# Optimization experiments

Measured on AMD Instinct MI355X. Metric: run time of the kernel, lower is better.

## Reference

```python
import jax, jax.numpy as jnp
import numpy as np

B, T, D = 4, 2048, 1024

def layer_norm(x, gamma, bias):
    # NOTE: faithfully reproduces the source's (buggy) LN: x - mu/sqrt(var), unbiased var
    mu = jnp.mean(x, axis=-1, keepdims=True)
    var = jnp.var(x, axis=-1, ddof=1, keepdims=True)
    return (x - mu / jnp.sqrt(var)) * gamma + bias

def setup_inputs() -> dict:
    key = jax.random.key(0)
    ks = jax.random.split(key, 8)
    scale = 1.0 / np.sqrt(D)
    return {
        'x': jax.random.normal(ks[0], (B, T, D), dtype=jnp.float32),
        'gamma1': jnp.ones((D,), jnp.float32),
        'beta1': jnp.zeros((D,), jnp.float32),
        'w_q': jax.random.uniform(ks[1], (D, D), jnp.float32, -scale, scale),
        'w_k': jax.random.uniform(ks[2], (D, D), jnp.float32, -scale, scale),
        'w_v': jax.random.uniform(ks[3], (D, D), jnp.float32, -scale, scale),
        'gamma2': jnp.ones((D,), jnp.float32),
        'beta2': jnp.zeros((D,), jnp.float32),
        'W1': jax.random.uniform(ks[4], (D, D), jnp.float32, -scale, scale),
        'b1': jnp.zeros((D,), jnp.float32),
        'W2': jax.random.uniform(ks[5], (D, D), jnp.float32, -scale, scale),
        'b2': jnp.zeros((D,), jnp.float32),
    }

def reference(x, gamma1, beta1, w_q, w_k, w_v, gamma2, beta2, W1, b1, W2, b2):
    d_model = x.shape[-1]
    t = x.shape[1]
    h = layer_norm(x, gamma1, beta1)
    q = jnp.einsum('btk,kd->btd', h, w_q)
    k = jnp.einsum('btk,kd->btd', h, w_k)
    v = jnp.einsum('btk,kd->btd', h, w_v)
    scale = 1.0 / jnp.sqrt(jnp.asarray(d_model, x.dtype))
    causal = jnp.tril(jnp.ones((t, t), dtype=bool))
    mask = jnp.where(causal, 0.0, -jnp.inf).astype(x.dtype)
    scores = jnp.einsum('bqd,bkd->bqk', q, k) * scale + mask
    attn = jax.nn.softmax(scores, axis=-1)
    y = jnp.einsum('bqt,btd->bqd', attn, v) + x
    h2 = layer_norm(y, gamma2, beta2)
    out = jnp.maximum(h2 @ W1 + b1, 0.0) @ W2 + b2
    return out + y
```

## Files before the change

kernel.cpp:

```cpp
#include <hip/hip_runtime.h>
#include <hip/hip_bf16.h>
#include <math.h>

using bf16 = __hip_bfloat16;

static constexpr int Bn = 4;
static constexpr int Tn = 2048;
static constexpr int Dn = 1024;

typedef __attribute__((ext_vector_type(8))) short bf16x8;
typedef __attribute__((ext_vector_type(4))) float f32x4;

__device__ __forceinline__ float ldf(float v) { return v; }
__device__ __forceinline__ float ldf(bf16 v) { return __bfloat162float(v); }
__device__ __forceinline__ bf16 f2b(float v) { return __float2bfloat16(v); }
__device__ __forceinline__ float b2f(short s) {
    return __uint_as_float(((unsigned)(unsigned short)s) << 16);
}
__device__ __forceinline__ short f2bs(float v) {
    bf16 t = __float2bfloat16(v);
    return *reinterpret_cast<short*>(&t);
}

template <typename T> __device__ __forceinline__ T from_float(float v);
template <> __device__ __forceinline__ float from_float<float>(float v) { return v; }
template <> __device__ __forceinline__ bf16 from_float<bf16>(float v) { return f2b(v); }

__device__ __forceinline__ void load4(const float* p, float* v) {
    const float4 t = *(const float4*)p;
    v[0] = t.x; v[1] = t.y; v[2] = t.z; v[3] = t.w;
}
__device__ __forceinline__ void load4(const bf16* p, float* v) {
    const short4 t = *(const short4*)p;
    v[0] = b2f(t.x); v[1] = b2f(t.y); v[2] = b2f(t.z); v[3] = b2f(t.w);
}

__device__ __forceinline__ void async_copy16(const bf16* g, bf16* l) {
    __builtin_amdgcn_global_load_lds(
        (const __attribute__((address_space(1))) void*)g,
        (__attribute__((address_space(3))) void*)l,
        16, 0, 0);
}

__global__ __launch_bounds__(512, 2) void gemm8p(
    const bf16* __restrict__ A, const bf16* __restrict__ Bm,
    bf16* __restrict__ C, int K, int lda, int ldb, int ldc)
{
    constexpr int BM = 256, BN = 256, BK = 32;
    constexpr int BUFE = (BM + BN) * BK;
    __shared__ __align__(16) bf16 smem[3 * BUFE];

    const int bm = blockIdx.x, bn = blockIdx.y;
    const int tid = threadIdx.x;
    const int wave = tid >> 6;
    const int lane = tid & 63;
    const int wm = wave >> 2;
    const int wn = wave & 3;
    const int lr = lane >> 2;
    const int lc = (lane & 3) * 8;
    const int arow = lane & 15;
    const int kq = (lane >> 4) * 8;

    const int NK = K / BK;

    const bf16* gA0 = A + (size_t)(bm * BM + wave * 16 + lr) * lda + lc;
    const bf16* gA1 = A + (size_t)(bm * BM + (wave + 8) * 16 + lr) * lda + lc;
    const bf16* gB0 = Bm + (size_t)(bn * BN + wave * 16 + lr) * ldb + lc;
    const bf16* gB1 = Bm + (size_t)(bn * BN + (wave + 8) * 16 + lr) * ldb + lc;

    f32x4 acc[8][4] = {};

    {
        bf16* As0 = smem;
        bf16* Bs0 = smem + BM * BK;
        bf16* As1 = smem + BUFE;
        bf16* Bs1 = smem + BUFE + BM * BK;
        async_copy16(gA0, As0 + wave * 512);
        async_copy16(gA1, As0 + (wave + 8) * 512);
        async_copy16(gB0, Bs0 + wave * 512);
        async_copy16(gB1, Bs0 + (wave + 8) * 512);
        async_copy16(gA0 + BK, As1 + wave * 512);
        async_copy16(gA1 + BK, As1 + (wave + 8) * 512);
        async_copy16(gB0 + BK, Bs1 + wave * 512);
        async_copy16(gB1 + BK, Bs1 + (wave + 8) * 512);
    }
    asm volatile("s_waitcnt vmcnt(4)" ::: "memory");
    __builtin_amdgcn_s_barrier();

    int cb = 0;
    int sb = 2;
    for (int kt = 0; kt < NK; ++kt) {
        const bf16* As = smem + cb * BUFE;
        const bf16* Bs = As + BM * BK;
        const bool st = (kt + 2) < NK;
        const int koff = (kt + 2) * BK;

        bf16x8 af[8], bf0[2];
#pragma unroll
        for (int mt = 0; mt < 8; ++mt)
            af[mt] = *(const bf16x8*)&As[(wm * 8 + mt) * 512 + arow * 32 + kq];
#pragma unroll
        for (int nt = 0; nt < 2; ++nt)
            bf0[nt] = *(const bf16x8*)&Bs[(wn * 4 + nt) * 512 + arow * 32 + kq];
        if (st) {
            bf16* Ad = smem + sb * BUFE;
            async_copy16(gA0 + koff, Ad + wave * 512);
            async_copy16(gA1 + koff, Ad + (wave + 8) * 512);
        }
        __builtin_amdgcn_s_barrier();
        asm volatile("s_waitcnt lgkmcnt(0)" ::: "memory");
        __builtin_amdgcn_sched_barrier(0);
        __builtin_amdgcn_s_setprio(1);
#pragma unroll
        for (int mt = 0; mt < 8; ++mt)
#pragma unroll
            for (int nt = 0; nt < 2; ++nt)
                acc[mt][nt] = __builtin_amdgcn_mfma_f32_16x16x32_bf16(
                    af[mt], bf0[nt], acc[mt][nt], 0, 0, 0);
        __builtin_amdgcn_s_setprio(0);
        __builtin_amdgcn_s_barrier();

        bf16x8 bf1[2];
#pragma unroll
        for (int nt = 0; nt < 2; ++nt)
            bf1[nt] = *(const bf16x8*)&Bs[(wn * 4 + 2 + nt) * 512 + arow * 32 + kq];
        if (st) {
            bf16* Bd = smem + sb * BUFE + BM * BK;
            async_copy16(gB0 + koff, Bd + wave * 512);
            async_copy16(gB1 + koff, Bd + (wave + 8) * 512);
        }
        __builtin_amdgcn_s_barrier();
        asm volatile("s_waitcnt lgkmcnt(0)" ::: "memory");
        __builtin_amdgcn_sched_barrier(0);
        __builtin_amdgcn_s_setprio(1);
#pragma unroll
        for (int mt = 0; mt < 8; ++mt)
#pragma unroll
            for (int nt = 0; nt < 2; ++nt)
                acc[mt][2 + nt] = __builtin_amdgcn_mfma_f32_16x16x32_bf16(
                    af[mt], bf1[nt], acc[mt][2 + nt], 0, 0, 0);
        __builtin_amdgcn_s_setprio(0);
        if (st) asm volatile("s_waitcnt vmcnt(4)" ::: "memory");
        else    asm volatile("s_waitcnt vmcnt(0)" ::: "memory");
        __builtin_amdgcn_s_barrier();

        cb = (cb + 1 == 3) ? 0 : cb + 1;
        sb = (sb + 1 == 3) ? 0 : sb + 1;
    }

    const int row0 = bm * BM + wm * 128;
    const int col0 = bn * BN + wn * 64;
    const int qrow = (lane >> 4) * 4;
    const int ccol = lane & 15;
#pragma unroll
    for (int mt = 0; mt < 8; ++mt)
#pragma unroll
        for (int nt = 0; nt < 4; ++nt) {
            const int cc = col0 + nt * 16 + ccol;
#pragma unroll
            for (int r = 0; r < 4; ++r) {
                const int rr = row0 + mt * 16 + qrow + r;
                C[(size_t)rr * ldc + cc] = f2b(acc[mt][nt][r]);
            }
        }
}

template <int BM, int BN, int MINW, int EPI, typename OutT, typename ResT, bool RELU>
__global__ __launch_bounds__(256, MINW) void gemm_nt(
    const bf16* __restrict__ A, const bf16* __restrict__ Bm,
    OutT* __restrict__ C, const float* __restrict__ bias,
    const ResT* __restrict__ res, bf16* __restrict__ vtp,
    float* __restrict__ rowsum,
    int M, int N, int K, int lda, int ldb, int ldc,
    long sA, long sB, long sC, long sR, int mode)
{
    const int bm = blockIdx.x, bn = blockIdx.y, bz = blockIdx.z;
    if (mode == 1 && bn * BN > bm * BM + (BM - 1)) return;
    const int kend = bm * BM + BM;
    const int kmax = (mode == 2) ? (kend < K ? kend : K) : K;

    const bf16* Ab = A + (size_t)bz * sA;
    const bf16* Bb = Bm + (size_t)bz * sB;

    constexpr int WROWS = BM / 64;
    constexpr int WCOLS = 4 / WROWS;
    constexpr int TM = 64;
    constexpr int TN = BN / WCOLS;
    constexpr int MT = TM / 16;
    constexpr int NT = TN / 16;
    constexpr int nA = BM / 16;
    constexpr int nB = BN / 16;
    constexpr int STAGE = 2 * (BM + BN) * 32;

    __shared__ __align__(16) bf16 smem[STAGE];
    bf16* As = smem;
    bf16* Bs = smem + 2 * BM * 32;

    const int tid = threadIdx.x;
    const int wave = tid >> 6;
    const int lane = tid & 63;
    const int wm = wave / WCOLS;
    const int wn = wave % WCOLS;

    f32x4 acc[MT][NT] = {};

    const int lr = lane >> 2;
    const int lc = (lane & 3) * 8;
    const bf16* gAc[nA / 4]; bf16* lAc[nA / 4];
    const bf16* gBc[nB / 4]; bf16* lBc[nB / 4];
#pragma unroll
    for (int i = 0; i < nA / 4; ++i) {
        const int c = wave + 4 * i;
        gAc[i] = Ab + (size_t)(bm * BM + c * 16 + lr) * lda + lc;
        lAc[i] = &As[c * 512];
    }
#pragma unroll
    for (int i = 0; i < nB / 4; ++i) {
        const int c = wave + 4 * i;
        gBc[i] = Bb + (size_t)(bn * BN + c * 16 + lr) * ldb + lc;
        lBc[i] = &Bs[c * 512];
    }

    const int arow = lane & 15;
    const int kq = (lane >> 4) * 8;

    for (int k0 = 0; k0 < kmax; k0 += 64) {
#pragma unroll
        for (int hh = 0; hh < 2; ++hh) {
#pragma unroll
            for (int i = 0; i < nA / 4; ++i)
                async_copy16(gAc[i] + k0 + 32 * hh, lAc[i] + hh * (BM * 32));
#pragma unroll
            for (int i = 0; i < nB / 4; ++i)
                async_copy16(gBc[i] + k0 + 32 * hh, lBc[i] + hh * (BN * 32));
        }
        __syncthreads();

#pragma unroll
        for (int hh = 0; hh < 2; ++hh) {
            const bf16* Ah = As + hh * (BM * 32);
            const bf16* Bh = Bs + hh * (BN * 32);
            bf16x8 af[MT], bfm[NT];
#pragma unroll
            for (int t = 0; t < MT; ++t)
                af[t] = *(const bf16x8*)&Ah[(wm * TM + t * 16 + arow) * 32 + kq];
#pragma unroll
            for (int t = 0; t < NT; ++t)
                bfm[t] = *(const bf16x8*)&Bh[(wn * TN + t * 16 + arow) * 32 + kq];
#pragma unroll
            for (int mt = 0; mt < MT; ++mt)
#pragma unroll
                for (int nt = 0; nt < NT; ++nt)
                    acc[mt][nt] = __builtin_amdgcn_mfma_f32_16x16x32_bf16(
                        af[mt], bfm[nt], acc[mt][nt], 0, 0, 0);
        }
        __syncthreads();
    }

    const int rowBase = bm * BM + wm * TM;
    const int colBase = bn * BN + wn * TN;
    const int qrow = (lane >> 4) * 4;
    const int ccol = lane & 15;

    if (EPI == 2) {
        OutT* Cb = C + (size_t)bz * sC;
        float* rsb = rowsum + (size_t)bz * Tn;
        const float scale = 0.03125f;
#pragma unroll
        for (int mt = 0; mt < MT; ++mt) {
            float rsv[4] = {0.f, 0.f, 0.f, 0.f};
#pragma unroll
            for (int nt = 0; nt < NT; ++nt) {
                const int cc = colBase + nt * 16 + ccol;
#pragma unroll
                for (int r = 0; r < 4; ++r) {
                    const int rr = rowBase + mt * 16 + qrow + r;
                    float e = 0.0f;
                    if (cc <= rr) {
                        const short es = f2bs(__expf(acc[mt][nt][r] * scale));
                        Cb[(size_t)rr * ldc + cc] = *(const bf16*)&es;
                        e = b2f(es);
                    } else {
                        Cb[(size_t)rr * ldc + cc] = from_float<OutT>(0.0f);
                    }
                    rsv[r] += e;
                }
            }
#pragma unroll
            for (int r = 0; r < 4; ++r) {
                float v = rsv[r];
                v += __shfl_xor(v, 1);
                v += __shfl_xor(v, 2);
                v += __shfl_xor(v, 4);
                v += __shfl_xor(v, 8);
                if (ccol == 0)
                    atomicAdd(rsb + rowBase + mt * 16 + qrow + r, v);
            }
        }
        return;
    }

    OutT* Cb = C + (size_t)bz * sC;
    const ResT* Rb = res ? (res + (size_t)bz * sR) : nullptr;
    const float* rsb = (EPI == 3) ? (rowsum + (size_t)bz * Tn) : nullptr;
#pragma unroll
    for (int mt = 0; mt < MT; ++mt) {
        float inv4[4];
        if (EPI == 3) {
#pragma unroll
            for (int r = 0; r < 4; ++r)
                inv4[r] = 1.0f / rsb[rowBase + mt * 16 + qrow + r];
        }
#pragma unroll
        for (int nt = 0; nt < NT; ++nt) {
            const int cc = colBase + nt * 16 + ccol;
            const float bv = bias ? bias[cc] : 0.0f;
#pragma unroll
            for (int r = 0; r < 4; ++r) {
                const int rr = rowBase + mt * 16 + qrow + r;
                float v = acc[mt][nt][r];
                if (EPI == 3) v *= inv4[r];
                v += bv;
                if (RELU) v = fmaxf(v, 0.0f);
                if (Rb) v += ldf(Rb[(size_t)rr * ldc + cc]);
                Cb[(size_t)rr * ldc + cc] = from_float<OutT>(v);
            }
        }
    }
}

template <typename InT>
__device__ __forceinline__ void ln_row(
    const InT* __restrict__ xr, const float* __restrict__ gamma,
    const float* __restrict__ beta, bf16* __restrict__ orow, int tid)
{
    const int j = tid * 4;
    float v[4];
    load4(xr + j, v);
    float s = v[0] + v[1] + v[2] + v[3];
    float sq = v[0] * v[0] + v[1] * v[1] + v[2] * v[2] + v[3] * v[3];
#pragma unroll
    for (int o = 32; o > 0; o >>= 1) {
        s += __shfl_down(s, o);
        sq += __shfl_down(sq, o);
    }
    __shared__ float red[2][4];
    const int lane = tid & 63, w = tid >> 6;
    if (lane == 0) { red[0][w] = s; red[1][w] = sq; }
    __syncthreads();
    s  = red[0][0] + red[0][1] + red[0][2] + red[0][3];
    sq = red[1][0] + red[1][1] + red[1][2] + red[1][3];
    const float mean = s / (float)Dn;
    const float var = (sq - s * s / (float)Dn) / (float)(Dn - 1);
    const float coef = mean * rsqrtf(var);

    const float4 g = *(const float4*)(gamma + j);
    const float4 be = *(const float4*)(beta + j);
    short4 o;
    o.x = f2bs((v[0] - coef) * g.x + be.x);
    o.y = f2bs((v[1] - coef) * g.y + be.y);
    o.z = f2bs((v[2] - coef) * g.z + be.z);
    o.w = f2bs((v[3] - coef) * g.w + be.w);
    *(short4*)(orow + j) = o;
}

template <typename InT>
__global__ __launch_bounds__(256) void ln_kernel(
    const InT* __restrict__ x, const float* __restrict__ gamma,
    const float* __restrict__ beta, bf16* __restrict__ out)
{
    const int row = blockIdx.x;
    ln_row(x + (size_t)row * Dn, gamma, beta, out + (size_t)row * Dn, threadIdx.x);
}

struct WPtrs { const float* p[5]; };

__global__ __launch_bounds__(256) void prep_kernel(
    WPtrs wp, bf16* __restrict__ wdst, float* __restrict__ rowsum,
    const float* __restrict__ x, const float* __restrict__ gamma1,
    const float* __restrict__ beta1, bf16* __restrict__ h)
{
    const int bx = blockIdx.x;
    if (bx < 5120) {
        __shared__ bf16 tile[32][33];
        const int z = bx >> 10;
        const int t = bx & 1023;
        const float* src = wp.p[z];
        bf16* d = wdst + (size_t)z * Dn * Dn;
        const int c0 = (t & 31) * 32, r0 = (t >> 5) * 32;
        const int tx = threadIdx.x & 31;
        const int ty = threadIdx.x >> 5;
#pragma unroll
        for (int dy = 0; dy < 32; dy += 8)
            tile[ty + dy][tx] = f2b(src[(size_t)(r0 + ty + dy) * Dn + (c0 + tx)]);
        __syncthreads();
#pragma unroll
        for (int dy = 0; dy < 32; dy += 8)
            d[(size_t)(c0 + ty + dy) * Dn + (r0 + tx)] = tile[tx][ty + dy];
    } else if (bx < 5128) {
        const int base = (bx - 5120) * 1024;
#pragma unroll
        for (int i = 0; i < 4; ++i) rowsum[base + i * 256 + threadIdx.x] = 0.0f;
    } else {
        const int row = bx - 5128;
        ln_row(x + (size_t)row * Dn, gamma1, beta1, h + (size_t)row * Dn, threadIdx.x);
    }
}

extern "C" void kernel_launch(void* const* d_in, const int* in_sizes, int n_in,
                              void* d_out, int out_size, void* d_ws, size_t ws_size,
                              hipStream_t stream) {
    const float* x      = (const float*)d_in[0];
    const float* gamma1 = (const float*)d_in[1];
    const float* beta1  = (const float*)d_in[2];
    const float* w_q    = (const float*)d_in[3];
    const float* w_k    = (const float*)d_in[4];
    const float* w_v    = (const float*)d_in[5];
    const float* gamma2 = (const float*)d_in[6];
    const float* beta2  = (const float*)d_in[7];
    const float* W1     = (const float*)d_in[8];
    const float* b1     = (const float*)d_in[9];
    const float* W2     = (const float*)d_in[10];
    const float* b2     = (const float*)d_in[11];
    float* out = (float*)d_out;

    char* ws = (char*)d_ws;
    size_t off = 0;
    auto alloc = [&](size_t bytes) {
        char* p = ws + off;
        off += (bytes + 255) & ~(size_t)255;
        return p;
    };
    const size_t BT = (size_t)Bn * Tn;
    bf16* h    = (bf16*)alloc(BT * Dn * 2);
    bf16* qk   = (bf16*)alloc(BT * 2 * Dn * 2);
    bf16* vt   = (bf16*)alloc(BT * Dn * 2);
    bf16* wbuf = (bf16*)alloc((size_t)5 * Dn * Dn * 2);
    bf16* S    = (bf16*)alloc((size_t)Bn * Tn * Tn * 2);
    bf16* y    = (bf16*)alloc(BT * Dn * 2);
    float* rowsum = (float*)alloc((size_t)Bn * Tn * 4);
    bf16* h2   = h;
    bf16* mid  = qk;

    const dim3 blk(256);
    const long TD  = (long)Tn * Dn;
    const long TT  = (long)Tn * Tn;
    const long TD2 = (long)Tn * 2 * Dn;

    WPtrs wp; wp.p[0] = w_q; wp.p[1] = w_k; wp.p[2] = w_v; wp.p[3] = W1; wp.p[4] = W2;
    prep_kernel<<<dim3(5128 + (unsigned)BT, 1, 1), blk, 0, stream>>>(
        wp, wbuf, rowsum, x, gamma1, beta1, h);

    gemm8p<<<dim3(32, 8, 1), dim3(512), 0, stream>>>(
        h, wbuf, qk, Dn, Dn, Dn, 2 * Dn);

    gemm_nt<128, 128, 4, 0, bf16, float, false><<<dim3(8, 16, Bn), blk, 0, stream>>>(
        wbuf + (size_t)2 * Dn * Dn, h, vt, nullptr, nullptr, nullptr, nullptr,
        Dn, Tn, Dn, Dn, Dn, Tn, 0, TD, (long)Dn * Tn, 0, 0);

    gemm_nt<128, 128, 4, 2, bf16, float, false><<<dim3(16, 16, Bn), blk, 0, stream>>>(
        qk, qk + 1024, S, nullptr, nullptr, nullptr, rowsum,
        Tn, Tn, Dn, 2 * Dn, 2 * Dn, Tn, TD2, TD2, TT, 0, 1);

    gemm_nt<128, 128, 4, 3, bf16, float, false><<<dim3(16, 8, Bn), blk, 0, stream>>>(
        S, vt, y, nullptr, x, nullptr, rowsum,
        Tn, Dn, Tn, Tn, Tn, Dn, TT, TD, TD, TD, 2);

    ln_kernel<bf16><<<dim3((unsigned)BT), blk, 0, stream>>>(y, gamma2, beta2, h2);

    gemm_nt<128, 128, 4, 0, bf16, float, true><<<dim3(64, 8, 1), blk, 0, stream>>>(
        h2, wbuf + (size_t)3 * Dn * Dn, mid, b1, nullptr, nullptr, nullptr,
        (int)BT, Dn, Dn, Dn, Dn, Dn, 0, 0, 0, 0, 0);

    gemm_nt<128, 128, 4, 0, float, bf16, false><<<dim3(64, 8, 1), blk, 0, stream>>>(
        mid, wbuf + (size_t)4 * Dn * Dn, out, b2, y, nullptr, nullptr,
        (int)BT, Dn, Dn, Dn, Dn, Dn, 0, 0, 0, 0, 0);
}
```

Measured before the change: 353.1 us.

## Generalize 8-wave pipelined GEMM and route V projection and MLP GEMMs through it

Templates the 512-thread triple-buffered gemm8p kernel on BN, epilogue type, output type and ReLU, and adds an epilogue with bias, ReLU and residual. The V projection now runs through this kernel with a 256x128 tile, transposing through shared memory to write V^T directly. The two MLP GEMMs move from the 128x128 gemm_nt kernel to the same 256x128 pipelined kernel. The aim is better MFMA utilization and more data reuse on these GEMMs. The risks are fewer blocks (256) for wave occupancy and a costlier LDS transpose epilogue.

```diff
diff --git a/kernel.cpp b/kernel.cpp
--- a/kernel.cpp
+++ b/kernel.cpp
@@ -42,11 +42,16 @@
         16, 0, 0);
 }
 
+template <int BN, int EPI, typename OutT, bool RELU>
 __global__ __launch_bounds__(512, 2) void gemm8p(
     const bf16* __restrict__ A, const bf16* __restrict__ Bm,
-    bf16* __restrict__ C, int K, int lda, int ldb, int ldc)
+    OutT* __restrict__ C, const float* __restrict__ bias,
+    const bf16* __restrict__ res, bf16* __restrict__ vtp,
+    int K, int lda, int ldb, int ldc)
 {
-    constexpr int BM = 256, BN = 256, BK = 32;
+    static_assert(EPI != 1 || BN == 128, "V-transpose epilogue needs BN=128");
+    constexpr int BM = 256, BK = 32;
+    constexpr int NT = BN / 64;
     constexpr int BUFE = (BM + BN) * BK;
     __shared__ __align__(16) bf16 smem[3 * BUFE];
 
@@ -66,9 +71,10 @@
     const bf16* gA0 = A + (size_t)(bm * BM + wave * 16 + lr) * lda + lc;
     const bf16* gA1 = A + (size_t)(bm * BM + (wave + 8) * 16 + lr) * lda + lc;
     const bf16* gB0 = Bm + (size_t)(bn * BN + wave * 16 + lr) * ldb + lc;
-    const bf16* gB1 = Bm + (size_t)(bn * BN + (wave + 8) * 16 + lr) * ldb + lc;
-
-    f32x4 acc[8][4] = {};
+    const bf16* gB1 = (BN == 256)
+        ? Bm + (size_t)(bn * BN + (wave + 8) * 16 + lr) * ldb + lc : nullptr;
+
+    f32x4 acc[8][NT] = {};
 
     {
         bf16* As0 = smem;
@@ -78,13 +84,14 @@
         async_copy16(gA0, As0 + wave * 512);
         async_copy16(gA1, As0 + (wave + 8) * 512);
         async_copy16(gB0, Bs0 + wave * 512);
-        async_copy16(gB1, Bs0 + (wave + 8) * 512);
+        if constexpr (BN == 256) async_copy16(gB1, Bs0 + (wave + 8) * 512);
         async_copy16(gA0 + BK, As1 + wave * 512);
         async_copy16(gA1 + BK, As1 + (wave + 8) * 512);
         async_copy16(gB0 + BK, Bs1 + wave * 512);
-        async_copy16(gB1 + BK, Bs1 + (wave + 8) * 512);
-    }
-    asm volatile("s_waitcnt vmcnt(4)" ::: "memory");
+        if constexpr (BN == 256) async_copy16(gB1 + BK, Bs1 + (wave + 8) * 512);
+    }
+    if constexpr (BN == 256) asm volatile("s_waitcnt vmcnt(4)" ::: "memory");
+    else                     asm volatile("s_waitcnt vmcnt(3)" ::: "memory");
     __builtin_amdgcn_s_barrier();
 
     int cb = 0;
@@ -95,13 +102,13 @@
         const bool st = (kt + 2) < NK;
         const int koff = (kt + 2) * BK;
 
-        bf16x8 af[8], bf0[2];
+        bf16x8 af[8], bf0[NT / 2];
 #pragma unroll
         for (int mt = 0; mt < 8; ++mt)
             af[mt] = *(const bf16x8*)&As[(wm * 8 + mt) * 512 + arow * 32 + kq];
 #pragma unroll
-        for (int nt = 0; nt < 2; ++nt)
-            bf0[nt] = *(const bf16x8*)&Bs[(wn * 4 + nt) * 512 + arow * 32 + kq];
+        for (int nt = 0; nt < NT / 2; ++nt)
+            bf0[nt] = *(const bf16x8*)&Bs[(wn * NT + nt) * 512 + arow * 32 + kq];
         if (st) {
             bf16* Ad = smem + sb * BUFE;
             async_copy16(gA0 + koff, Ad + wave * 512);
@@ -114,20 +121,20 @@
 #pragma unroll
         for (int mt = 0; mt < 8; ++mt)
 #pragma unroll
-            for (int nt = 0; nt < 2; ++nt)
+            for (int nt = 0; nt < NT / 2; ++nt)
                 acc[mt][nt] = __builtin_amdgcn_mfma_f32_16x16x32_bf16(
                     af[mt], bf0[nt], acc[mt][nt], 0, 0, 0);
         __builtin_amdgcn_s_setprio(0);
         __builtin_amdgcn_s_barrier();
 
-        bf16x8 bf1[2];
-#pragma unroll
-        for (int nt = 0; nt < 2; ++nt)
-            bf1[nt] = *(const bf16x8*)&Bs[(wn * 4 + 2 + nt) * 512 + arow * 32 + kq];
+        bf16x8 bf1[NT / 2];
+#pragma unroll
+        for (int nt = 0; nt < NT / 2; ++nt)
+            bf1[nt] = *(const bf16x8*)&Bs[(wn * NT + NT / 2 + nt) * 512 + arow * 32 + kq];
         if (st) {
             bf16* Bd = smem + sb * BUFE + BM * BK;
             async_copy16(gB0 + koff, Bd + wave * 512);
-            async_copy16(gB1 + koff, Bd + (wave + 8) * 512);
+            if constexpr (BN == 256) async_copy16(gB1 + koff, Bd + (wave + 8) * 512);
         }
         __builtin_amdgcn_s_barrier();
         asm volatile("s_waitcnt lgkmcnt(0)" ::: "memory");
@@ -136,31 +143,71 @@
 #pragma unroll
         for (int mt = 0; mt < 8; ++mt)
 #pragma unroll
-            for (int nt = 0; nt < 2; ++nt)
-                acc[mt][2 + nt] = __builtin_amdgcn_mfma_f32_16x16x32_bf16(
-                    af[mt], bf1[nt], acc[mt][2 + nt], 0, 0, 0);
+            for (int nt = 0; nt < NT / 2; ++nt)
+                acc[mt][NT / 2 + nt] = __builtin_amdgcn_mfma_f32_16x16x32_bf16(
+                    af[mt], bf1[nt], acc[mt][NT / 2 + nt], 0, 0, 0);
         __builtin_amdgcn_s_setprio(0);
-        if (st) asm volatile("s_waitcnt vmcnt(4)" ::: "memory");
-        else    asm volatile("s_waitcnt vmcnt(0)" ::: "memory");
+        if (st) {
+            if constexpr (BN == 256) asm volatile("s_waitcnt vmcnt(4)" ::: "memory");
+            else                     asm volatile("s_waitcnt vmcnt(3)" ::: "memory");
+        } else {
+            asm volatile("s_waitcnt vmcnt(0)" ::: "memory");
+        }
         __builtin_amdgcn_s_barrier();
 
         cb = (cb + 1 == 3) ? 0 : cb + 1;
         sb = (sb + 1 == 3) ? 0 : sb + 1;
     }
 
-    const int row0 = bm * BM + wm * 128;
-    const int col0 = bn * BN + wn * 64;
     const int qrow = (lane >> 4) * 4;
     const int ccol = lane & 15;
+
+    if constexpr (EPI == 1) {
+        bf16* tt = smem;
+#pragma unroll
+        for (int mt = 0; mt < 8; ++mt)
+#pragma unroll
+            for (int nt = 0; nt < NT; ++nt) {
+                const int dl = wn * (NT * 16) + nt * 16 + ccol;
+                const int tl = wm * 128 + mt * 16 + qrow;
+                short4 o;
+                o.x = f2bs(acc[mt][nt][0]);
+                o.y = f2bs(acc[mt][nt][1]);
+                o.z = f2bs(acc[mt][nt][2]);
+                o.w = f2bs(acc[mt][nt][3]);
+                *(short4*)&tt[dl * 264 + tl] = o;
+            }
+        __syncthreads();
+        const int b = (bm * BM) >> 11;
+        const int tin = (bm * BM) & (Tn - 1);
+        const int dr = tid >> 4;
+        const int t0 = (tid & 15) * 16;
+#pragma unroll
+        for (int p = 0; p < 4; ++p) {
+            const int d = p * 32 + dr;
+            const bf16* srcl = &tt[d * 264 + t0];
+            bf16* dst = vtp + ((size_t)b * Dn + bn * BN + d) * Tn + tin + t0;
+            ((bf16x8*)dst)[0] = ((const bf16x8*)srcl)[0];
+            ((bf16x8*)dst)[1] = ((const bf16x8*)srcl)[1];
+        }
+        return;
+    }
+
+    const int row0 = bm * BM + wm * 128;
+    const int col0 = bn * BN + wn * (NT * 16);
 #pragma unroll
     for (int mt = 0; mt < 8; ++mt)
 #pragma unroll
-        for (int nt = 0; nt < 4; ++nt) {
+        for (int nt = 0; nt < NT; ++nt) {
             const int cc = col0 + nt * 16 + ccol;
+            const float bv = bias ? bias[cc] : 0.0f;
 #pragma unroll
             for (int r = 0; r < 4; ++r) {
                 const int rr = row0 + mt * 16 + qrow + r;
-                C[(size_t)rr * ldc + cc] = f2b(acc[mt][nt][r]);
+                float v = acc[mt][nt][r] + bv;
+                if (RELU) v = fmaxf(v, 0.0f);
+                if (res) v += b2f(*(const short*)&res[(size_t)rr * ldc + cc]);
+                C[(size_t)rr * ldc + cc] = from_float<OutT>(v);
             }
         }
 }
@@ -451,12 +498,12 @@
     prep_kernel<<<dim3(5128 + (unsigned)BT, 1, 1), blk, 0, stream>>>(
         wp, wbuf, rowsum, x, gamma1, beta1, h);
 
-    gemm8p<<<dim3(32, 8, 1), dim3(512), 0, stream>>>(
-        h, wbuf, qk, Dn, Dn, Dn, 2 * Dn);
-
-    gemm_nt<128, 128, 4, 0, bf16, float, false><<<dim3(8, 16, Bn), blk, 0, stream>>>(
-        wbuf + (size_t)2 * Dn * Dn, h, vt, nullptr, nullptr, nullptr, nullptr,
-        Dn, Tn, Dn, Dn, Dn, Tn, 0, TD, (long)Dn * Tn, 0, 0);
+    gemm8p<256, 0, bf16, false><<<dim3(32, 8, 1), dim3(512), 0, stream>>>(
+        h, wbuf, qk, nullptr, nullptr, nullptr, Dn, Dn, Dn, 2 * Dn);
+
+    gemm8p<128, 1, bf16, false><<<dim3(32, 8, 1), dim3(512), 0, stream>>>(
+        h, wbuf + (size_t)2 * Dn * Dn, (bf16*)nullptr, nullptr, nullptr, vt,
+        Dn, Dn, Dn, 0);
 
     gemm_nt<128, 128, 4, 2, bf16, float, false><<<dim3(16, 16, Bn), blk, 0, stream>>>(
         qk, qk + 1024, S, nullptr, nullptr, nullptr, rowsum,
@@ -468,11 +515,11 @@
 
     ln_kernel<bf16><<<dim3((unsigned)BT), blk, 0, stream>>>(y, gamma2, beta2, h2);
 
-    gemm_nt<128, 128, 4, 0, bf16, float, true><<<dim3(64, 8, 1), blk, 0, stream>>>(
-        h2, wbuf + (size_t)3 * Dn * Dn, mid, b1, nullptr, nullptr, nullptr,
-        (int)BT, Dn, Dn, Dn, Dn, Dn, 0, 0, 0, 0, 0);
-
-    gemm_nt<128, 128, 4, 0, float, bf16, false><<<dim3(64, 8, 1), blk, 0, stream>>>(
-        mid, wbuf + (size_t)4 * Dn * Dn, out, b2, y, nullptr, nullptr,
-        (int)BT, Dn, Dn, Dn, Dn, Dn, 0, 0, 0, 0, 0);
-}
+    gemm8p<128, 0, bf16, true><<<dim3(32, 8, 1), dim3(512), 0, stream>>>(
+        h2, wbuf + (size_t)3 * Dn * Dn, mid, b1, nullptr, nullptr,
+        Dn, Dn, Dn, Dn);
+
+    gemm8p<128, 0, float, false><<<dim3(32, 8, 1), dim3(512), 0, stream>>>(
+        mid, wbuf + (size_t)4 * Dn * Dn, out, b2, y, nullptr,
+        Dn, Dn, Dn, Dn);
+}
```

After: 362.5 us. +2.7%, slower.

## Replace generic GEMMs with 8-wave 256x128 triple-buffered pipelined kernel

Applied to the files above, without the earlier changes.

Replaces the 256-thread gemm_nt, which synchronises twice per k-step and does no prefetch, with a 512-thread 256x128-tile kernel. The new kernel uses three shared-memory buffers with async copies issued two k-steps ahead, split A/B staging, and raised wave priority around the MFMA blocks. It hides global-load latency and improves reuse for the V projection, the attention score, PV and both FFN GEMMs. The V projection now computes h·Wv in normal orientation and writes the transpose through an LDS tile in its epilogue. Larger tiles halve the grid sizes, which may hurt load balance on the causal triangle, and the 96KB-plus shared memory limits occupancy.

```diff
diff --git a/kernel.cpp b/kernel.cpp
--- a/kernel.cpp
+++ b/kernel.cpp
@@ -87,8 +87,7 @@
     asm volatile("s_waitcnt vmcnt(4)" ::: "memory");
     __builtin_amdgcn_s_barrier();
 
-    int cb = 0;
-    int sb = 2;
+    int cb = 0, sb = 2;
     for (int kt = 0; kt < NK; ++kt) {
         const bf16* As = smem + cb * BUFE;
         const bf16* Bs = As + BM * BK;
@@ -165,116 +164,166 @@
         }
 }
 
-template <int BM, int BN, int MINW, int EPI, typename OutT, typename ResT, bool RELU>
-__global__ __launch_bounds__(256, MINW) void gemm_nt(
+template <int EPI, int MODE, typename OutT, typename ResT, bool RELU>
+__global__ __launch_bounds__(512, 2) void gemm8k(
     const bf16* __restrict__ A, const bf16* __restrict__ Bm,
     OutT* __restrict__ C, const float* __restrict__ bias,
     const ResT* __restrict__ res, bf16* __restrict__ vtp,
     float* __restrict__ rowsum,
-    int M, int N, int K, int lda, int ldb, int ldc,
-    long sA, long sB, long sC, long sR, int mode)
+    int K, int lda, int ldb, int ldc, int ldr,
+    long sA, long sB, long sC, long sR)
 {
+    constexpr int BM = 256, BN = 128;
+    constexpr int AE = BM * 32;
+    constexpr int BE = BN * 32;
+    constexpr int BUFE = 2 * (AE + BE);
+    __shared__ __align__(16) bf16 smem[3 * BUFE];
+
     const int bm = blockIdx.x, bn = blockIdx.y, bz = blockIdx.z;
-    if (mode == 1 && bn * BN > bm * BM + (BM - 1)) return;
+    if (MODE == 1 && bn * BN > bm * BM + (BM - 1)) return;
     const int kend = bm * BM + BM;
-    const int kmax = (mode == 2) ? (kend < K ? kend : K) : K;
+    const int kmax = (MODE == 2) ? (kend < K ? kend : K) : K;
+    const int NK = kmax >> 6;
 
     const bf16* Ab = A + (size_t)bz * sA;
     const bf16* Bb = Bm + (size_t)bz * sB;
-
-    constexpr int WROWS = BM / 64;
-    constexpr int WCOLS = 4 / WROWS;
-    constexpr int TM = 64;
-    constexpr int TN = BN / WCOLS;
-    constexpr int MT = TM / 16;
-    constexpr int NT = TN / 16;
-    constexpr int nA = BM / 16;
-    constexpr int nB = BN / 16;
-    constexpr int STAGE = 2 * (BM + BN) * 32;
-
-    __shared__ __align__(16) bf16 smem[STAGE];
-    bf16* As = smem;
-    bf16* Bs = smem + 2 * BM * 32;
 
     const int tid = threadIdx.x;
     const int wave = tid >> 6;
     const int lane = tid & 63;
-    const int wm = wave / WCOLS;
-    const int wn = wave % WCOLS;
-
-    f32x4 acc[MT][NT] = {};
-
+    const int wm = wave >> 2;
+    const int wn = wave & 3;
     const int lr = lane >> 2;
     const int lc = (lane & 3) * 8;
-    const bf16* gAc[nA / 4]; bf16* lAc[nA / 4];
-    const bf16* gBc[nB / 4]; bf16* lBc[nB / 4];
-#pragma unroll
-    for (int i = 0; i < nA / 4; ++i) {
-        const int c = wave + 4 * i;
-        gAc[i] = Ab + (size_t)(bm * BM + c * 16 + lr) * lda + lc;
-        lAc[i] = &As[c * 512];
-    }
-#pragma unroll
-    for (int i = 0; i < nB / 4; ++i) {
-        const int c = wave + 4 * i;
-        gBc[i] = Bb + (size_t)(bn * BN + c * 16 + lr) * ldb + lc;
-        lBc[i] = &Bs[c * 512];
-    }
-
     const int arow = lane & 15;
     const int kq = (lane >> 4) * 8;
 
-    for (int k0 = 0; k0 < kmax; k0 += 64) {
-#pragma unroll
-        for (int hh = 0; hh < 2; ++hh) {
-#pragma unroll
-            for (int i = 0; i < nA / 4; ++i)
-                async_copy16(gAc[i] + k0 + 32 * hh, lAc[i] + hh * (BM * 32));
-#pragma unroll
-            for (int i = 0; i < nB / 4; ++i)
-                async_copy16(gBc[i] + k0 + 32 * hh, lBc[i] + hh * (BN * 32));
-        }
-        __syncthreads();
-
-#pragma unroll
-        for (int hh = 0; hh < 2; ++hh) {
-            const bf16* Ah = As + hh * (BM * 32);
-            const bf16* Bh = Bs + hh * (BN * 32);
-            bf16x8 af[MT], bfm[NT];
-#pragma unroll
-            for (int t = 0; t < MT; ++t)
-                af[t] = *(const bf16x8*)&Ah[(wm * TM + t * 16 + arow) * 32 + kq];
-#pragma unroll
-            for (int t = 0; t < NT; ++t)
-                bfm[t] = *(const bf16x8*)&Bh[(wn * TN + t * 16 + arow) * 32 + kq];
-#pragma unroll
-            for (int mt = 0; mt < MT; ++mt)
-#pragma unroll
-                for (int nt = 0; nt < NT; ++nt)
-                    acc[mt][nt] = __builtin_amdgcn_mfma_f32_16x16x32_bf16(
-                        af[mt], bfm[nt], acc[mt][nt], 0, 0, 0);
-        }
-        __syncthreads();
-    }
-
-    const int rowBase = bm * BM + wm * TM;
-    const int colBase = bn * BN + wn * TN;
+    const bf16* gA0 = Ab + (size_t)(bm * BM + wave * 16 + lr) * lda + lc;
+    const bf16* gA1 = Ab + (size_t)(bm * BM + (wave + 8) * 16 + lr) * lda + lc;
+    const bf16* gB0 = Bb + (size_t)(bn * BN + wave * 16 + lr) * ldb + lc;
+
+    f32x4 acc[8][2] = {};
+
+    auto stageA = [&](bf16* buf, int k0) {
+        async_copy16(gA0 + k0,      buf + wave * 512);
+        async_copy16(gA1 + k0,      buf + (wave + 8) * 512);
+        async_copy16(gA0 + k0 + 32, buf + AE + wave * 512);
+        async_copy16(gA1 + k0 + 32, buf + AE + (wave + 8) * 512);
+    };
+    auto stageB = [&](bf16* buf, int k0) {
+        async_copy16(gB0 + k0,      buf + 2 * AE + wave * 512);
+        async_copy16(gB0 + k0 + 32, buf + 2 * AE + BE + wave * 512);
+    };
+
+    stageA(smem, 0);        stageB(smem, 0);
+    stageA(smem + BUFE, 64); stageB(smem + BUFE, 64);
+    asm volatile("s_waitcnt vmcnt(6)" ::: "memory");
+    __builtin_amdgcn_s_barrier();
+
+    int cb = 0, sb = 2;
+    for (int kt = 0; kt < NK; ++kt) {
+        const bf16* As = smem + cb * BUFE;
+        const bf16* Bs = As + 2 * AE;
+        const bool st = (kt + 2) < NK;
+        const int koff = (kt + 2) * 64;
+
+        bf16x8 af[8], bfr[2];
+#pragma unroll
+        for (int mt = 0; mt < 8; ++mt)
+            af[mt] = *(const bf16x8*)&As[(wm * 8 + mt) * 512 + arow * 32 + kq];
+#pragma unroll
+        for (int nt = 0; nt < 2; ++nt)
+            bfr[nt] = *(const bf16x8*)&Bs[(wn * 2 + nt) * 512 + arow * 32 + kq];
+        if (st) stageA(smem + sb * BUFE, koff);
+        __builtin_amdgcn_s_barrier();
+        asm volatile("s_waitcnt lgkmcnt(0)" ::: "memory");
+        __builtin_amdgcn_sched_barrier(0);
+        __builtin_amdgcn_s_setprio(1);
+#pragma unroll
+        for (int mt = 0; mt < 8; ++mt)
+#pragma unroll
+            for (int nt = 0; nt < 2; ++nt)
+                acc[mt][nt] = __builtin_amdgcn_mfma_f32_16x16x32_bf16(
+                    af[mt], bfr[nt], acc[mt][nt], 0, 0, 0);
+        __builtin_amdgcn_s_setprio(0);
+        __builtin_amdgcn_s_barrier();
+
+        bf16x8 af2[8], bfr2[2];
+#pragma unroll
+        for (int mt = 0; mt < 8; ++mt)
+            af2[mt] = *(const bf16x8*)&As[AE + (wm * 8 + mt) * 512 + arow * 32 + kq];
+#pragma unroll
+        for (int nt = 0; nt < 2; ++nt)
+            bfr2[nt] = *(const bf16x8*)&Bs[BE + (wn * 2 + nt) * 512 + arow * 32 + kq];
+        if (st) stageB(smem + sb * BUFE, koff);
+        __builtin_amdgcn_s_barrier();
+        asm volatile("s_waitcnt lgkmcnt(0)" ::: "memory");
+        __builtin_amdgcn_sched_barrier(0);
+        __builtin_amdgcn_s_setprio(1);
+#pragma unroll
+        for (int mt = 0; mt < 8; ++mt)
+#pragma unroll
+            for (int nt = 0; nt < 2; ++nt)
+                acc[mt][nt] = __builtin_amdgcn_mfma_f32_16x16x32_bf16(
+                    af2[mt], bfr2[nt], acc[mt][nt], 0, 0, 0);
+        __builtin_amdgcn_s_setprio(0);
+        if (st) asm volatile("s_waitcnt vmcnt(6)" ::: "memory");
+        else    asm volatile("s_waitcnt vmcnt(0)" ::: "memory");
+        __builtin_amdgcn_s_barrier();
+
+        cb = (cb + 1 == 3) ? 0 : cb + 1;
+        sb = (sb + 1 == 3) ? 0 : sb + 1;
+    }
+
     const int qrow = (lane >> 4) * 4;
     const int ccol = lane & 15;
-
-    if (EPI == 2) {
+    const int row0 = bm * BM + wm * 128;
+    const int col0 = bn * BN + wn * 32;
+
+    if constexpr (EPI == 1) {
+        bf16* tt = smem;
+#pragma unroll
+        for (int mt = 0; mt < 8; ++mt)
+#pragma unroll
+            for (int nt = 0; nt < 2; ++nt) {
+                const int dl = wn * 32 + nt * 16 + ccol;
+                const int tl = wm * 128 + mt * 16 + qrow;
+                short4 o;
+                o.x = f2bs(acc[mt][nt][0]);
+                o.y = f2bs(acc[mt][nt][1]);
+                o.z = f2bs(acc[mt][nt][2]);
+                o.w = f2bs(acc[mt][nt][3]);
+                *(short4*)&tt[dl * 264 + tl] = o;
+            }
+        __syncthreads();
+        const int b = (bm * BM) >> 11;
+        const int tin = (bm * BM) & (Tn - 1);
+        const int dr = tid >> 4;
+        const int t0 = (tid & 15) * 16;
+#pragma unroll
+        for (int p = 0; p < 4; ++p) {
+            const int d = p * 32 + dr;
+            const bf16* srcl = &tt[d * 264 + t0];
+            bf16* dst = vtp + ((size_t)b * Dn + bn * BN + d) * Tn + tin + t0;
+            ((bf16x8*)dst)[0] = ((const bf16x8*)srcl)[0];
+            ((bf16x8*)dst)[1] = ((const bf16x8*)srcl)[1];
+        }
+        return;
+    }
+
+    if constexpr (EPI == 2) {
         OutT* Cb = C + (size_t)bz * sC;
         float* rsb = rowsum + (size_t)bz * Tn;
         const float scale = 0.03125f;
 #pragma unroll
-        for (int mt = 0; mt < MT; ++mt) {
+        for (int mt = 0; mt < 8; ++mt) {
             float rsv[4] = {0.f, 0.f, 0.f, 0.f};
 #pragma unroll
-            for (int nt = 0; nt < NT; ++nt) {
-                const int cc = colBase + nt * 16 + ccol;
+            for (int nt = 0; nt < 2; ++nt) {
+                const int cc = col0 + nt * 16 + ccol;
 #pragma unroll
                 for (int r = 0; r < 4; ++r) {
-                    const int rr = rowBase + mt * 16 + qrow + r;
+                    const int rr = row0 + mt * 16 + qrow + r;
                     float e = 0.0f;
                     if (cc <= rr) {
                         const short es = f2bs(__expf(acc[mt][nt][r] * scale));
@@ -294,7 +343,7 @@
                 v += __shfl_xor(v, 4);
                 v += __shfl_xor(v, 8);
                 if (ccol == 0)
-                    atomicAdd(rsb + rowBase + mt * 16 + qrow + r, v);
+                    atomicAdd(rsb + row0 + mt * 16 + qrow + r, v);
             }
         }
         return;
@@ -304,25 +353,25 @@
     const ResT* Rb = res ? (res + (size_t)bz * sR) : nullptr;
     const float* rsb = (EPI == 3) ? (rowsum + (size_t)bz * Tn) : nullptr;
 #pragma unroll
-    for (int mt = 0; mt < MT; ++mt) {
+    for (int mt = 0; mt < 8; ++mt) {
         float inv4[4];
-        if (EPI == 3) {
+        if constexpr (EPI == 3) {
 #pragma unroll
             for (int r = 0; r < 4; ++r)
-                inv4[r] = 1.0f / rsb[rowBase + mt * 16 + qrow + r];
-        }
-#pragma unroll
-        for (int nt = 0; nt < NT; ++nt) {
-            const int cc = colBase + nt * 16 + ccol;
+                inv4[r] = 1.0f / rsb[row0 + mt * 16 + qrow + r];
+        }
+#pragma unroll
+        for (int nt = 0; nt < 2; ++nt) {
+            const int cc = col0 + nt * 16 + ccol;
             const float bv = bias ? bias[cc] : 0.0f;
 #pragma unroll
             for (int r = 0; r < 4; ++r) {
-                const int rr = rowBase + mt * 16 + qrow + r;
+                const int rr = row0 + mt * 16 + qrow + r;
                 float v = acc[mt][nt][r];
-                if (EPI == 3) v *= inv4[r];
+                if constexpr (EPI == 3) v *= inv4[r];
                 v += bv;
                 if (RELU) v = fmaxf(v, 0.0f);
-                if (Rb) v += ldf(Rb[(size_t)rr * ldc + cc]);
+                if (Rb) v += ldf(Rb[(size_t)rr * ldr + cc]);
                 Cb[(size_t)rr * ldc + cc] = from_float<OutT>(v);
             }
         }
@@ -443,36 +492,38 @@
     bf16* mid  = qk;
 
     const dim3 blk(256);
+    const dim3 blk512(512);
     const long TD  = (long)Tn * Dn;
     const long TT  = (long)Tn * Tn;
     const long TD2 = (long)Tn * 2 * Dn;
+    const size_t DD = (size_t)Dn * Dn;
 
     WPtrs wp; wp.p[0] = w_q; wp.p[1] = w_k; wp.p[2] = w_v; wp.p[3] = W1; wp.p[4] = W2;
     prep_kernel<<<dim3(5128 + (unsigned)BT, 1, 1), blk, 0, stream>>>(
         wp, wbuf, rowsum, x, gamma1, beta1, h);
 
-    gemm8p<<<dim3(32, 8, 1), dim3(512), 0, stream>>>(
+    gemm8p<<<dim3(32, 8, 1), blk512, 0, stream>>>(
         h, wbuf, qk, Dn, Dn, Dn, 2 * Dn);
 
-    gemm_nt<128, 128, 4, 0, bf16, float, false><<<dim3(8, 16, Bn), blk, 0, stream>>>(
-        wbuf + (size_t)2 * Dn * Dn, h, vt, nullptr, nullptr, nullptr, nullptr,
-        Dn, Tn, Dn, Dn, Dn, Tn, 0, TD, (long)Dn * Tn, 0, 0);
-
-    gemm_nt<128, 128, 4, 2, bf16, float, false><<<dim3(16, 16, Bn), blk, 0, stream>>>(
+    gemm8k<1, 0, bf16, float, false><<<dim3(32, 8, 1), blk512, 0, stream>>>(
+        h, wbuf + 2 * DD, (bf16*)nullptr, nullptr, nullptr, vt, nullptr,
+        Dn, Dn, Dn, 0, 0, 0, 0, 0, 0);
+
+    gemm8k<2, 1, bf16, float, false><<<dim3(8, 16, Bn), blk512, 0, stream>>>(
         qk, qk + 1024, S, nullptr, nullptr, nullptr, rowsum,
-        Tn, Tn, Dn, 2 * Dn, 2 * Dn, Tn, TD2, TD2, TT, 0, 1);
-
-    gemm_nt<128, 128, 4, 3, bf16, float, false><<<dim3(16, 8, Bn), blk, 0, stream>>>(
+        Dn, 2 * Dn, 2 * Dn, Tn, 0, TD2, TD2, TT, 0);
+
+    gemm8k<3, 2, bf16, float, false><<<dim3(8, 8, Bn), blk512, 0, stream>>>(
         S, vt, y, nullptr, x, nullptr, rowsum,
-        Tn, Dn, Tn, Tn, Tn, Dn, TT, TD, TD, TD, 2);
+        Tn, Tn, Tn, Dn, Dn, TT, TD, TD, TD);
 
     ln_kernel<bf16><<<dim3((unsigned)BT), blk, 0, stream>>>(y, gamma2, beta2, h2);
 
-    gemm_nt<128, 128, 4, 0, bf16, float, true><<<dim3(64, 8, 1), blk, 0, stream>>>(
-        h2, wbuf + (size_t)3 * Dn * Dn, mid, b1, nullptr, nullptr, nullptr,
-        (int)BT, Dn, Dn, Dn, Dn, Dn, 0, 0, 0, 0, 0);
-
-    gemm_nt<128, 128, 4, 0, float, bf16, false><<<dim3(64, 8, 1), blk, 0, stream>>>(
-        mid, wbuf + (size_t)4 * Dn * Dn, out, b2, y, nullptr, nullptr,
-        (int)BT, Dn, Dn, Dn, Dn, Dn, 0, 0, 0, 0, 0);
-}
+    gemm8k<0, 0, bf16, float, true><<<dim3(32, 8, 1), blk512, 0, stream>>>(
+        h2, wbuf + 3 * DD, mid, b1, nullptr, nullptr, nullptr,
+        Dn, Dn, Dn, Dn, 0, 0, 0, 0, 0);
+
+    gemm8k<0, 0, float, bf16, false><<<dim3(32, 8, 1), blk512, 0, stream>>>(
+        mid, wbuf + 4 * DD, out, b2, y, nullptr, nullptr,
+        Dn, Dn, Dn, Dn, Dn, 0, 0, 0, 0);
+}
```

New measurement: 391.9 us. 1.11x slower.
